# Kernel optimization log

Measured on AMD Instinct MI355X. Metric: run time of the kernel, lower is better.

## Reference

```python
import jax, jax.numpy as jnp
import numpy as np

EPS = 1e-5

def _bn(x, g, b, m, v):
    # eval-mode BatchNorm1d over channel dim of [B, C, T]
    scale = g / jnp.sqrt(v + EPS)
    return (x - m[:, None]) * scale[:, None] + b[:, None]

def _conv3(x, w, b):
    # [B, W, T] conv with kernel [W, W, 3], padding=1
    y = jax.lax.conv_general_dilated(x, w, (1,), [(1, 1)],
                                     dimension_numbers=('NCH', 'OIH', 'NCH'))
    return y + b[None, :, None]

def setup_inputs() -> dict:
    key = jax.random.key(0)
    ks = iter(jax.random.split(key, 32))
    def n(shape, s=0.05):
        return jax.random.normal(next(ks), shape, jnp.float32) * s
    def u(shape):
        return jax.random.uniform(next(ks), shape, jnp.float32, 0.5, 1.5)
    B, T, C, S, W = 128, 4096, 125, 5, 25
    return dict(
        low_freq=jax.random.normal(next(ks), (B, 10, T), jnp.float32),
        w1=n((S, W, 2)), b1=n((S, W)),
        w3=n((S - 1, W, W, 3)), b3=n((S - 1, W)),
        bn_g=jnp.ones((S, W)), bn_b=jnp.zeros((S, W)), bn_m=n((S, W)), bn_v=u((S, W)),
        gw1=n((C // 4, C)), gb1=n((C // 4,)),          # gating Linear(125, 31)
        gw2=n((S, C // 4)), gb2=n((S,)),               # gating Linear(31, 5)
        id_w=n((C, 10)), id_b=n((C,)),                 # identity_proj Conv1d(10,125,1)
        pf_w=n((C, C)), pf_b=n((C,)),                  # proj_final Conv1d(125,125,1)
        fbn_g=jnp.ones((C,)), fbn_b=jnp.zeros((C,)), fbn_m=n((C,)), fbn_v=u((C,)),
        ln_g=jnp.ones((C,)), ln_b=jnp.zeros((C,)),
        fc1_w=n((64, C)), fc1_b=n((64,)),
        fc2_w=n((2, 64)), fc2_b=n((2,)),
    )

def reference(low_freq, w1, b1, w3, b3, bn_g, bn_b, bn_m, bn_v,
              gw1, gb1, gw2, gb2, id_w, id_b, pf_w, pf_b,
              fbn_g, fbn_b, fbn_m, fbn_v, ln_g, ln_b,
              fc1_w, fc1_b, fc2_w, fc2_b):
    S = w1.shape[0]
    B, _, T = low_freq.shape
    identity = jnp.einsum('bct,oc->bot', low_freq, id_w) + id_b[None, :, None]
    chunks = low_freq.reshape(B, S, 2, T)              # torch.chunk over 10 channels
    # all 1x1 convs at once: [S, B, W, T]
    xs = jnp.einsum('bsct,swc->sbwt', chunks, w1) + b1[:, None, :, None]
    y = [None] * S
    y[S - 1] = jax.nn.relu(_bn(xs[S - 1], bn_g[S - 1], bn_b[S - 1], bn_m[S - 1], bn_v[S - 1]))
    for i in range(S - 2, -1, -1):                     # sequential Res2Net recursion
        yi = _conv3(xs[i] + y[i + 1], w3[i], b3[i])
        y[i] = jax.nn.relu(_bn(yi, bn_g[i], bn_b[i], bn_m[i], bn_v[i]))
    ms = jnp.concatenate(y, axis=1)                    # [B, 125, T]
    avg = jnp.mean(ms, axis=-1)                        # [B, 125]
    gate = jax.nn.sigmoid(jax.nn.relu(avg @ gw1.T + gb1) @ gw2.T + gb2)  # [B, S]
    yw = jnp.stack(y, axis=1) * gate[:, :, None, None] # [B, S, W, T]
    gated = yw.reshape(B, -1, T)
    proj = jnp.einsum('bct,oc->bot', gated, pf_w) + pf_b[None, :, None]
    out = jax.nn.relu(_bn(proj + identity, fbn_g, fbn_b, fbn_m, fbn_v))
    pooled = jnp.mean(out, axis=-1)                    # GAP -> [B, 125]
    mu = jnp.mean(pooled, axis=-1, keepdims=True)
    var = jnp.var(pooled, axis=-1, keepdims=True)
    normed = (pooled - mu) / jnp.sqrt(var + EPS) * ln_g + ln_b
    h = normed @ fc1_w.T + fc1_b
    h = jnp.where(h > 0, h, 0.2 * h)                   # LeakyReLU(0.2); dropout = identity (eval)
    return h @ fc2_w.T + fc2_b                         # [B, 2]
```

## Files before the change

kernel.cpp:

```cpp
#include <hip/hip_runtime.h>
#include <stdint.h>

typedef unsigned short u16;
typedef unsigned int   u32;
using short8 = __attribute__((ext_vector_type(8))) short;
using f32x4  = __attribute__((ext_vector_type(4))) float;

__device__ __forceinline__ u16 f2bf(float f){
  u32 u = __builtin_bit_cast(u32, f);
  u = u + 0x7fffu + ((u >> 16) & 1u);
  return (u16)(u >> 16);
}
__device__ __forceinline__ u32 packbf2(float a, float b){
  u32 ua = __builtin_bit_cast(u32, a) + 0x8000u;
  u32 ub = __builtin_bit_cast(u32, b) + 0x8000u;
  return (ua >> 16) | (ub & 0xffff0000u);
}

__global__ void prep_kernel(const float* __restrict__ w3,
                            const float* __restrict__ w1,
                            const float* __restrict__ b1,
                            const float* __restrict__ bng,
                            const float* __restrict__ bnv,
                            u16* __restrict__ convA)
{
  int idx = blockIdx.x*256 + threadIdx.x;
  if (idx >= 4*2*3*64*8) return;
  int j = idx & 7, l = (idx>>3) & 63, frag = idx >> 9;
  int tap = frag % 3, mt = (frag/3) & 1, lay = frag/6;
  int m = mt*16 + (l & 15);
  int k = (l>>4)*8 + j;
  float v = 0.f;
  if (m < 25){
    float a = bng[lay*25+m] * rsqrtf(bnv[lay*25+m] + 1e-5f);
    if (k < 25){
      v = a * w3[((lay*25+m)*25 + k)*3 + tap];
    } else if (k == 25){
      float s = 0.f;
      for (int c = 0; c < 25; ++c) s += w3[((lay*25+m)*25+c)*3+tap] * b1[lay*25+c];
      v = a * s;
    } else if (k <= 27){
      int e = k - 26;
      float s = 0.f;
      for (int c = 0; c < 25; ++c) s += w3[((lay*25+m)*25+c)*3+tap] * w1[(lay*25+c)*2+e];
      v = a * s;
    }
  }
  convA[idx] = f2bf(v);
}

template<int PASS>
__global__ __launch_bounds__(256, (PASS==1) ? 3 : 2)
void pass_kernel(const float* __restrict__ lfg,
                 const float* __restrict__ w1g, const float* __restrict__ b1g,
                 const float* __restrict__ b3g,
                 const float* __restrict__ bng, const float* __restrict__ bnb,
                 const float* __restrict__ bnm, const float* __restrict__ bnv,
                 const u16* __restrict__ convA, const u16* __restrict__ Ab,
                 const float* __restrict__ pfb, const float* __restrict__ idb,
                 const float* __restrict__ fbg, const float* __restrict__ fbb,
                 const float* __restrict__ fbm, const float* __restrict__ fbv,
                 float* __restrict__ outpart)
{
  constexpr int CZ = 66;
  __shared__ __align__(16) u16 zws[4][2][CZ*40];
  __shared__ __align__(16) float cAs[4][32];
  __shared__ __align__(16) float w4as[32], w4bs[32], c4s[32];
  __shared__ float accC[(PASS==1)?160:4];
  __shared__ __align__(16) float AfS[(PASS==2)?128:4], BfS[(PASS==2)?128:4];

  const int tid  = threadIdx.x;
  const int lane = tid & 63, wv = tid >> 6;
  const int q = lane >> 4, c16 = lane & 15;
  const int b = blockIdx.y, blk = blockIdx.x;
  const int s = blk*4 + wv;
  const int tbase = s*32 - 16;

  for (int x = tid; x < 4*2*CZ*20; x += 256) ((u32*)zws)[x] = 0u;
  __syncthreads();
  for (int x = tid; x < 4*2*CZ; x += 256){
    int w = x/(2*CZ), rb = (x/CZ)&1, cz = x%CZ;
    int t = (blk*4+w)*32 - 16 + cz - 1;
    zws[w][rb][cz*40 + 25] = ((unsigned)t < 4096u) ? (u16)0x3F80 : (u16)0;
  }
  if (tid < 128){
    int i = tid >> 5, ch = tid & 31;
    float cc = 0.f;
    if (ch < 25){
      float a = bng[i*25+ch]*rsqrtf(bnv[i*25+ch]+1e-5f);
      cc = (b3g[i*25+ch] - bnm[i*25+ch])*a + bnb[i*25+ch];
    }
    cAs[i][ch] = cc;
  } else if (tid < 160){
    int ch = tid - 128;
    float wa=0.f, wb=0.f, cf=0.f;
    if (ch < 25){
      float a = bng[100+ch]*rsqrtf(bnv[100+ch]+1e-5f);
      wa = a*w1g[(100+ch)*2+0]; wb = a*w1g[(100+ch)*2+1];
      cf = a*b1g[100+ch] + (bnb[100+ch] - bnm[100+ch]*a);
    }
    w4as[ch]=wa; w4bs[ch]=wb; c4s[ch]=cf;
  }
  if constexpr (PASS==1){ if (tid < 160) accC[tid] = 0.f; }
  if constexpr (PASS==2){
    if (tid < 128){
      float fs=0.f, fsh=0.f;
      if (tid < 125){
        fs  = fbg[tid]*rsqrtf(fbv[tid]+1e-5f);
        fsh = (pfb[tid]+idb[tid]-fbm[tid])*fs + fbb[tid];
      }
      AfS[tid]=fs; BfS[tid]=fsh;
    }
  }
  __syncthreads();

  const float* lfb = lfg + b*10*4096;

  u32 lpair[4];
  {
    int t = tbase + lane;
    bool ok = (unsigned)t < 4096u;
    #pragma unroll
    for (int k = 0; k < 4; ++k){
      float a = ok ? lfb[(2*k  )*4096 + t] : 0.f;
      float c = ok ? lfb[(2*k+1)*4096 + t] : 0.f;
      lpair[k] = packbf2(a, c);
    }
  }

  f32x4 pacc[2][8];
  if constexpr (PASS==2){
    #pragma unroll
    for (int n2=0;n2<2;++n2)
      #pragma unroll
      for (int m2=0;m2<8;++m2) pacc[n2][m2] = (f32x4){0.f,0.f,0.f,0.f};
  }

  u16* bufA = zws[wv][0];

  {
    const f32x4 wa0 = *(const f32x4*)&w4as[4*q];
    const f32x4 wa1 = *(const f32x4*)&w4as[16+4*q];
    const f32x4 wb0 = *(const f32x4*)&w4bs[4*q];
    const f32x4 wb1 = *(const f32x4*)&w4bs[16+4*q];
    const f32x4 cf0 = *(const f32x4*)&c4s[4*q];
    const f32x4 cf1 = *(const f32x4*)&c4s[16+4*q];
    float s4[8];
    #pragma unroll
    for (int e=0;e<8;++e) s4[e] = 0.f;
    #pragma unroll
    for (int ct=0; ct<4; ++ct){
      const int wc = 16*ct + c16;
      const int t  = tbase + wc;
      const bool tok = (unsigned)t < 4096u;
      const float l8 = tok ? lfb[8*4096 + t] : 0.f;
      const float l9 = tok ? lfb[9*4096 + t] : 0.f;
      float y0[4], y1[4];
      #pragma unroll
      for (int r=0;r<4;++r){
        float a = fmaxf(wa0[r]*l8 + wb0[r]*l9 + cf0[r], 0.f);
        float c = fmaxf(wa1[r]*l8 + wb1[r]*l9 + cf1[r], 0.f);
        y0[r] = tok ? a : 0.f;
        y1[r] = tok ? c : 0.f;
      }
      if (PASS==1 && (ct==1 || ct==2)){
        #pragma unroll
        for (int r=0;r<4;++r){ s4[r] += y0[r]; s4[4+r] += y1[r]; }
      }
      uint2 w0; w0.x = packbf2(y0[0],y0[1]); w0.y = packbf2(y0[2],y0[3]);
      *(uint2*)&bufA[(wc+1)*40 + 4*q] = w0;
      if (q < 2){
        uint2 w1_; w1_.x = packbf2(y1[0],y1[1]); w1_.y = packbf2(y1[2],y1[3]);
        *(uint2*)&bufA[(wc+1)*40 + 16 + 4*q] = w1_;
      } else if (q == 2){
        bufA[(wc+1)*40 + 24] = f2bf(y1[0]);
      }
    }
    *(u32*)&bufA[(lane+1)*40 + 26] = lpair[3];
    if constexpr (PASS==1){
      #pragma unroll
      for (int e=0;e<8;++e){
        float v = s4[e];
        v += __shfl_xor(v,1); v += __shfl_xor(v,2); v += __shfl_xor(v,4); v += __shfl_xor(v,8);
        if (c16 == 0){
          int ch = (e>>2)*16 + 4*q + (e&3);
          if (ch < 25) atomicAdd(&accC[4*32+ch], v);
        }
      }
    }
  }

  if constexpr (PASS==2){
    {
      short8 Am[8];
      #pragma unroll
      for (int m2=0;m2<8;++m2)
        Am[m2] = *(const short8*)(Ab + b*24576 + ((4*8+m2)*64 + lane)*8);
      #pragma unroll
      for (int n2=0;n2<2;++n2){
        const short8 Bm = *(const short8*)&bufA[(17+16*n2+c16)*40 + 8*q];
        #pragma unroll
        for (int m2=0;m2<8;++m2)
          pacc[n2][m2] = __builtin_amdgcn_mfma_f32_16x16x32_bf16(Am[m2], Bm, pacc[n2][m2],0,0,0);
      }
    }
    {
      short8 Am[8];
      #pragma unroll
      for (int m2=0;m2<8;++m2)
        Am[m2] = *(const short8*)(Ab + b*24576 + ((5*8+m2)*64 + lane)*8);
      #pragma unroll
      for (int n2=0;n2<2;++n2){
        const int t = tbase + 16 + 16*n2 + c16;
        u32 bw[4];
        #pragma unroll
        for (int p=0;p<4;++p){
          int k0 = 8*q + 2*p;
          float v0 = (k0   < 10) ? lfb[k0*4096 + t] : 0.f;
          float v1 = (k0+1 < 10) ? lfb[(k0+1)*4096 + t] : 0.f;
          bw[p] = packbf2(v0, v1);
        }
        const short8 Bm = __builtin_bit_cast(short8, bw);
        #pragma unroll
        for (int m2=0;m2<8;++m2)
          pacc[n2][m2] = __builtin_amdgcn_mfma_f32_16x16x32_bf16(Am[m2], Bm, pacc[n2][m2],0,0,0);
      }
    }
  }

  #pragma unroll
  for (int i = 3; i >= 0; --i){
    u16* src = zws[wv][(3-i)&1];
    u16* dst = zws[wv][(4-i)&1];
    short8 Ac0[3], Ac1[3];
    #pragma unroll
    for (int tp=0;tp<3;++tp){
      Ac0[tp] = *(const short8*)(convA + (((i*2+0)*3+tp)*64 + lane)*8);
      Ac1[tp] = *(const short8*)(convA + (((i*2+1)*3+tp)*64 + lane)*8);
    }
    const f32x4 cc0 = *(const f32x4*)&cAs[i][4*q];
    const f32x4 cc1 = *(const f32x4*)&cAs[i][16+4*q];
    float ysum[8];
    #pragma unroll
    for (int e=0;e<8;++e) ysum[e] = 0.f;

    #pragma unroll
    for (int ct=0; ct<4; ++ct){
      const int wc = 16*ct + c16;
      const u16* p = src + wc*40 + 8*q;
      short8 t0 = *(const short8*)(p);
      short8 t1 = *(const short8*)(p + 40);
      short8 t2 = *(const short8*)(p + 80);
      f32x4 a0 = {0.f,0.f,0.f,0.f}, a1 = {0.f,0.f,0.f,0.f};
      a0 = __builtin_amdgcn_mfma_f32_16x16x32_bf16(Ac0[0], t0, a0, 0,0,0);
      a1 = __builtin_amdgcn_mfma_f32_16x16x32_bf16(Ac1[0], t0, a1, 0,0,0);
      a0 = __builtin_amdgcn_mfma_f32_16x16x32_bf16(Ac0[1], t1, a0, 0,0,0);
      a1 = __builtin_amdgcn_mfma_f32_16x16x32_bf16(Ac1[1], t1, a1, 0,0,0);
      a0 = __builtin_amdgcn_mfma_f32_16x16x32_bf16(Ac0[2], t2, a0, 0,0,0);
      a1 = __builtin_amdgcn_mfma_f32_16x16x32_bf16(Ac1[2], t2, a1, 0,0,0);
      const int t = tbase + wc;
      const bool tok = (unsigned)t < 4096u;
      float y0[4], y1[4];
      #pragma unroll
      for (int r=0;r<4;++r){
        float u0 = fmaxf(a0[r] + cc0[r], 0.f);
        float u1 = fmaxf(a1[r] + cc1[r], 0.f);
        y0[r] = tok ? u0 : 0.f;
        y1[r] = tok ? u1 : 0.f;
      }
      if (PASS==1 && (ct==1 || ct==2)){
        #pragma unroll
        for (int r=0;r<4;++r){ ysum[r] += y0[r]; ysum[4+r] += y1[r]; }
      }
      uint2 w0; w0.x = packbf2(y0[0],y0[1]); w0.y = packbf2(y0[2],y0[3]);
      *(uint2*)&dst[(wc+1)*40 + 4*q] = w0;
      if (q < 2){
        uint2 w1_; w1_.x = packbf2(y1[0],y1[1]); w1_.y = packbf2(y1[2],y1[3]);
        *(uint2*)&dst[(wc+1)*40 + 16 + 4*q] = w1_;
      } else if (q == 2){
        dst[(wc+1)*40 + 24] = f2bf(y1[0]);
      }
    }
    if (i > 0) *(u32*)&dst[(lane+1)*40 + 26] = lpair[i-1];
    if constexpr (PASS==1){
      #pragma unroll
      for (int e=0;e<8;++e){
        float v = ysum[e];
        v += __shfl_xor(v,1); v += __shfl_xor(v,2); v += __shfl_xor(v,4); v += __shfl_xor(v,8);
        if (c16 == 0){
          int ch = (e>>2)*16 + 4*q + (e&3);
          if (ch < 25) atomicAdd(&accC[i*32+ch], v);
        }
      }
    }
    if constexpr (PASS==2){
      short8 Am[8];
      #pragma unroll
      for (int m2=0;m2<8;++m2)
        Am[m2] = *(const short8*)(Ab + b*24576 + ((i*8+m2)*64 + lane)*8);
      #pragma unroll
      for (int n2=0;n2<2;++n2){
        const short8 Bm = *(const short8*)&dst[(17+16*n2+c16)*40 + 8*q];
        #pragma unroll
        for (int m2=0;m2<8;++m2)
          pacc[n2][m2] = __builtin_amdgcn_mfma_f32_16x16x32_bf16(Am[m2], Bm, pacc[n2][m2],0,0,0);
      }
    }
  }

  if constexpr (PASS==1){
    __syncthreads();
    if (tid < 160) outpart[(b*32 + blk)*160 + tid] = accC[tid];
  }
  if constexpr (PASS==2){
    f32x4 ps[8];
    #pragma unroll
    for (int m2=0;m2<8;++m2){
      const f32x4 af = *(const f32x4*)&AfS[m2*16+4*q];
      const f32x4 bf = *(const f32x4*)&BfS[m2*16+4*q];
      #pragma unroll
      for (int r=0;r<4;++r){
        float s2 = fmaxf(pacc[0][m2][r]*af[r] + bf[r], 0.f)
                 + fmaxf(pacc[1][m2][r]*af[r] + bf[r], 0.f);
        s2 += __shfl_xor(s2,1); s2 += __shfl_xor(s2,2); s2 += __shfl_xor(s2,4); s2 += __shfl_xor(s2,8);
        ps[m2][r] = s2;
      }
    }
    if (c16 == 0){
      const int widx = (b*32 + blk)*4 + wv;
      #pragma unroll
      for (int m2=0;m2<8;++m2)
        *(f32x4*)&outpart[widx*128 + m2*16 + 4*q] = ps[m2];
    }
  }
}

__global__ void gate_kernel(const float* __restrict__ partialC,
                            const float* __restrict__ gw1, const float* __restrict__ gb1,
                            const float* __restrict__ gw2, const float* __restrict__ gb2,
                            const float* __restrict__ pf_w, const float* __restrict__ id_w,
                            u16* __restrict__ Ab)
{
  int b = blockIdx.x, tid = threadIdx.x;
  __shared__ float avg[125], h1[31], g[6];
  if (tid < 160){
    float s = 0.f;
    for (int k = 0; k < 32; ++k) s += partialC[(b*32+k)*160 + tid];
    int sc = tid >> 5, ch = tid & 31;
    if (ch < 25) avg[sc*25+ch] = s * (1.f/4096.f);
  }
  __syncthreads();
  if (tid < 31){
    float s = gb1[tid];
    for (int c = 0; c < 125; ++c) s += avg[c] * gw1[tid*125 + c];
    h1[tid] = fmaxf(s, 0.f);
  }
  __syncthreads();
  if (tid < 5){
    float s = gb2[tid];
    for (int j = 0; j < 31; ++j) s += h1[j] * gw2[tid*31 + j];
    g[tid] = 1.f / (1.f + expf(-s));
  }
  if (tid == 5) g[5] = 1.f;
  __syncthreads();
  for (int idx = tid; idx < 24576; idx += 256){
    int j = idx & 7, l = (idx>>3) & 63, mt = (idx>>9) & 7, kt = idx >> 12;
    int m = mt*16 + (l & 15), k = (l>>4)*8 + j;
    float v = 0.f;
    if (m < 125){
      if (kt < 5){ if (k < 25) v = pf_w[m*125 + kt*25 + k] * g[kt]; }
      else       { if (k < 10) v = id_w[m*10 + k]; }
    }
    Ab[b*24576 + idx] = f2bf(v);
  }
}

__global__ void final_kernel(const float* __restrict__ pooledpart,
                             const float* __restrict__ ln_g, const float* __restrict__ ln_b,
                             const float* __restrict__ fc1_w, const float* __restrict__ fc1_b,
                             const float* __restrict__ fc2_w, const float* __restrict__ fc2_b,
                             float* __restrict__ out)
{
  int b = blockIdx.x, tid = threadIdx.x;
  __shared__ float pl[125], nr[125], hh[64], st[2];
  for (int c = tid; c < 125; c += 64){
    float s = 0.f;
    for (int k = 0; k < 128; ++k) s += pooledpart[(b*128+k)*128 + c];
    pl[c] = s * (1.f/4096.f);
  }
  __syncthreads();
  if (tid == 0){
    float mu = 0.f;
    for (int c = 0; c < 125; ++c) mu += pl[c];
    mu /= 125.f;
    float va = 0.f;
    for (int c = 0; c < 125; ++c){ float d = pl[c] - mu; va += d*d; }
    va /= 125.f;
    st[0] = mu; st[1] = rsqrtf(va + 1e-5f);
  }
  __syncthreads();
  for (int c = tid; c < 125; c += 64)
    nr[c] = (pl[c] - st[0]) * st[1] * ln_g[c] + ln_b[c];
  __syncthreads();
  {
    float s = fc1_b[tid];
    for (int c = 0; c < 125; ++c) s += nr[c] * fc1_w[tid*125 + c];
    hh[tid] = (s > 0.f) ? s : 0.2f * s;
  }
  __syncthreads();
  if (tid < 2){
    float s = fc2_b[tid];
    for (int j = 0; j < 64; ++j) s += hh[j] * fc2_w[tid*64 + j];
    out[b*2 + tid] = s;
  }
}

extern "C" void kernel_launch(void* const* d_in, const int* in_sizes, int n_in,
                              void* d_out, int out_size, void* d_ws, size_t ws_size,
                              hipStream_t stream)
{
  const float* lf    = (const float*)d_in[0];
  const float* w1    = (const float*)d_in[1];
  const float* b1    = (const float*)d_in[2];
  const float* w3    = (const float*)d_in[3];
  const float* b3    = (const float*)d_in[4];
  const float* bn_g  = (const float*)d_in[5];
  const float* bn_b  = (const float*)d_in[6];
  const float* bn_m  = (const float*)d_in[7];
  const float* bn_v  = (const float*)d_in[8];
  const float* gw1   = (const float*)d_in[9];
  const float* gb1   = (const float*)d_in[10];
  const float* gw2   = (const float*)d_in[11];
  const float* gb2   = (const float*)d_in[12];
  const float* id_w  = (const float*)d_in[13];
  const float* id_b  = (const float*)d_in[14];
  const float* pf_w  = (const float*)d_in[15];
  const float* pf_b  = (const float*)d_in[16];
  const float* fbn_g = (const float*)d_in[17];
  const float* fbn_b = (const float*)d_in[18];
  const float* fbn_m = (const float*)d_in[19];
  const float* fbn_v = (const float*)d_in[20];
  const float* ln_g  = (const float*)d_in[21];
  const float* ln_b  = (const float*)d_in[22];
  const float* fc1_w = (const float*)d_in[23];
  const float* fc1_b = (const float*)d_in[24];
  const float* fc2_w = (const float*)d_in[25];
  const float* fc2_b = (const float*)d_in[26];

  char* ws = (char*)d_ws;
  float* partialC   = (float*)ws;
  float* pooledpart = (float*)(ws + 2621440);
  u16*   Ab         = (u16*)(ws + 2621440 + 8388608);
  u16*   convA      = (u16*)(ws + 2621440 + 8388608 + 6291456);

  prep_kernel<<<48, 256, 0, stream>>>(w3, w1, b1, bn_g, bn_v, convA);
  pass_kernel<1><<<dim3(32,128), 256, 0, stream>>>(lf, w1, b1, b3, bn_g, bn_b,
      bn_m, bn_v, convA, Ab, pf_b, id_b, fbn_g, fbn_b, fbn_m, fbn_v, partialC);
  gate_kernel<<<128, 256, 0, stream>>>(partialC, gw1, gb1, gw2, gb2, pf_w, id_w, Ab);
  pass_kernel<2><<<dim3(32,128), 256, 0, stream>>>(lf, w1, b1, b3, bn_g, bn_b,
      bn_m, bn_v, convA, Ab, pf_b, id_b, fbn_g, fbn_b, fbn_m, fbn_v, pooledpart);
  final_kernel<<<128, 64, 0, stream>>>(pooledpart, ln_g, ln_b, fc1_w, fc1_b,
      fc2_w, fc2_b, (float*)d_out);
}
```

Measured before the change: 397.2 us.

## Single-buffer conv tiles with register prefetch, block-level pooling, parallel gate and final kernels

Each wave now keeps one LDS tile instead of a ping-pong pair and runs the conv recursion in place. The input fragments are prefetched into registers one column tile ahead, so LDS reads overlap the MFMA chain, and the bias constant is folded into the accumulator init. Pass 1 is asked to fit four blocks per CU instead of three. Pass 2 reduces its pooled sums inside the block through LDS atomics, which shrinks the partial buffer and the work left for the final kernel. The gate kernel is split across six blocks per batch, and the final kernel uses 256 threads with shuffle reductions. The in-place tile relies on wave-synchronous ordering of reads before writes, and the higher occupancy target could cause register spills.

```diff
diff --git a/kernel.cpp b/kernel.cpp
--- a/kernel.cpp
+++ b/kernel.cpp
@@ -50,7 +50,7 @@
 }
 
 template<int PASS>
-__global__ __launch_bounds__(256, (PASS==1) ? 3 : 2)
+__global__ __launch_bounds__(256, (PASS==1) ? 4 : 2)
 void pass_kernel(const float* __restrict__ lfg,
                  const float* __restrict__ w1g, const float* __restrict__ b1g,
                  const float* __restrict__ b3g,
@@ -63,10 +63,11 @@
                  float* __restrict__ outpart)
 {
   constexpr int CZ = 66;
-  __shared__ __align__(16) u16 zws[4][2][CZ*40];
+  __shared__ __align__(16) u16 zws[4][CZ*40];
   __shared__ __align__(16) float cAs[4][32];
   __shared__ __align__(16) float w4as[32], w4bs[32], c4s[32];
   __shared__ float accC[(PASS==1)?160:4];
+  __shared__ float pooled[(PASS==2)?128:4];
   __shared__ __align__(16) float AfS[(PASS==2)?128:4], BfS[(PASS==2)?128:4];
 
   const int tid  = threadIdx.x;
@@ -76,12 +77,12 @@
   const int s = blk*4 + wv;
   const int tbase = s*32 - 16;
 
-  for (int x = tid; x < 4*2*CZ*20; x += 256) ((u32*)zws)[x] = 0u;
-  __syncthreads();
-  for (int x = tid; x < 4*2*CZ; x += 256){
-    int w = x/(2*CZ), rb = (x/CZ)&1, cz = x%CZ;
+  for (int x = tid; x < 4*CZ*20; x += 256) ((u32*)zws)[x] = 0u;
+  __syncthreads();
+  for (int x = tid; x < 4*CZ; x += 256){
+    int w = x/CZ, cz = x%CZ;
     int t = (blk*4+w)*32 - 16 + cz - 1;
-    zws[w][rb][cz*40 + 25] = ((unsigned)t < 4096u) ? (u16)0x3F80 : (u16)0;
+    zws[w][cz*40 + 25] = ((unsigned)t < 4096u) ? (u16)0x3F80 : (u16)0;
   }
   if (tid < 128){
     int i = tid >> 5, ch = tid & 31;
@@ -104,6 +105,7 @@
   if constexpr (PASS==1){ if (tid < 160) accC[tid] = 0.f; }
   if constexpr (PASS==2){
     if (tid < 128){
+      pooled[tid] = 0.f;
       float fs=0.f, fsh=0.f;
       if (tid < 125){
         fs  = fbg[tid]*rsqrtf(fbv[tid]+1e-5f);
@@ -136,7 +138,7 @@
       for (int m2=0;m2<8;++m2) pacc[n2][m2] = (f32x4){0.f,0.f,0.f,0.f};
   }
 
-  u16* bufA = zws[wv][0];
+  u16* z = zws[wv];
 
   {
     const f32x4 wa0 = *(const f32x4*)&w4as[4*q];
@@ -168,15 +170,15 @@
         for (int r=0;r<4;++r){ s4[r] += y0[r]; s4[4+r] += y1[r]; }
       }
       uint2 w0; w0.x = packbf2(y0[0],y0[1]); w0.y = packbf2(y0[2],y0[3]);
-      *(uint2*)&bufA[(wc+1)*40 + 4*q] = w0;
+      *(uint2*)&z[(wc+1)*40 + 4*q] = w0;
       if (q < 2){
         uint2 w1_; w1_.x = packbf2(y1[0],y1[1]); w1_.y = packbf2(y1[2],y1[3]);
-        *(uint2*)&bufA[(wc+1)*40 + 16 + 4*q] = w1_;
+        *(uint2*)&z[(wc+1)*40 + 16 + 4*q] = w1_;
       } else if (q == 2){
-        bufA[(wc+1)*40 + 24] = f2bf(y1[0]);
-      }
-    }
-    *(u32*)&bufA[(lane+1)*40 + 26] = lpair[3];
+        z[(wc+1)*40 + 24] = f2bf(y1[0]);
+      }
+    }
+    *(u32*)&z[(lane+1)*40 + 26] = lpair[3];
     if constexpr (PASS==1){
       #pragma unroll
       for (int e=0;e<8;++e){
@@ -198,7 +200,7 @@
         Am[m2] = *(const short8*)(Ab + b*24576 + ((4*8+m2)*64 + lane)*8);
       #pragma unroll
       for (int n2=0;n2<2;++n2){
-        const short8 Bm = *(const short8*)&bufA[(17+16*n2+c16)*40 + 8*q];
+        const short8 Bm = *(const short8*)&z[(17+16*n2+c16)*40 + 8*q];
         #pragma unroll
         for (int m2=0;m2<8;++m2)
           pacc[n2][m2] = __builtin_amdgcn_mfma_f32_16x16x32_bf16(Am[m2], Bm, pacc[n2][m2],0,0,0);
@@ -230,8 +232,6 @@
 
   #pragma unroll
   for (int i = 3; i >= 0; --i){
-    u16* src = zws[wv][(3-i)&1];
-    u16* dst = zws[wv][(4-i)&1];
     short8 Ac0[3], Ac1[3];
     #pragma unroll
     for (int tp=0;tp<3;++tp){
@@ -244,27 +244,43 @@
     #pragma unroll
     for (int e=0;e<8;++e) ysum[e] = 0.f;
 
+    short8 F0[3], F1[3], F2[3];
+    {
+      const u16* p = z + c16*40 + 8*q;
+      F0[0] = *(const short8*)(p);
+      F0[1] = *(const short8*)(p + 40);
+      F0[2] = *(const short8*)(p + 80);
+      const u16* p1 = z + (16 + c16)*40 + 8*q;
+      F1[0] = *(const short8*)(p1);
+      F1[1] = *(const short8*)(p1 + 40);
+      F1[2] = *(const short8*)(p1 + 80);
+    }
     #pragma unroll
     for (int ct=0; ct<4; ++ct){
+      short8* cur = (ct==0) ? F0 : (ct==1) ? F1 : (ct==2) ? F2 : F0;
+      if (ct < 2){
+        short8* nxt = (ct==0) ? F2 : F0;
+        const u16* p = z + (16*(ct+2) + c16)*40 + 8*q;
+        nxt[0] = *(const short8*)(p);
+        nxt[1] = *(const short8*)(p + 40);
+        nxt[2] = *(const short8*)(p + 80);
+      }
+      __builtin_amdgcn_sched_barrier(0);
+      f32x4 a0 = cc0, a1 = cc1;
+      a0 = __builtin_amdgcn_mfma_f32_16x16x32_bf16(Ac0[0], cur[0], a0, 0,0,0);
+      a1 = __builtin_amdgcn_mfma_f32_16x16x32_bf16(Ac1[0], cur[0], a1, 0,0,0);
+      a0 = __builtin_amdgcn_mfma_f32_16x16x32_bf16(Ac0[1], cur[1], a0, 0,0,0);
+      a1 = __builtin_amdgcn_mfma_f32_16x16x32_bf16(Ac1[1], cur[1], a1, 0,0,0);
+      a0 = __builtin_amdgcn_mfma_f32_16x16x32_bf16(Ac0[2], cur[2], a0, 0,0,0);
+      a1 = __builtin_amdgcn_mfma_f32_16x16x32_bf16(Ac1[2], cur[2], a1, 0,0,0);
       const int wc = 16*ct + c16;
-      const u16* p = src + wc*40 + 8*q;
-      short8 t0 = *(const short8*)(p);
-      short8 t1 = *(const short8*)(p + 40);
-      short8 t2 = *(const short8*)(p + 80);
-      f32x4 a0 = {0.f,0.f,0.f,0.f}, a1 = {0.f,0.f,0.f,0.f};
-      a0 = __builtin_amdgcn_mfma_f32_16x16x32_bf16(Ac0[0], t0, a0, 0,0,0);
-      a1 = __builtin_amdgcn_mfma_f32_16x16x32_bf16(Ac1[0], t0, a1, 0,0,0);
-      a0 = __builtin_amdgcn_mfma_f32_16x16x32_bf16(Ac0[1], t1, a0, 0,0,0);
-      a1 = __builtin_amdgcn_mfma_f32_16x16x32_bf16(Ac1[1], t1, a1, 0,0,0);
-      a0 = __builtin_amdgcn_mfma_f32_16x16x32_bf16(Ac0[2], t2, a0, 0,0,0);
-      a1 = __builtin_amdgcn_mfma_f32_16x16x32_bf16(Ac1[2], t2, a1, 0,0,0);
-      const int t = tbase + wc;
+      const int t  = tbase + wc;
       const bool tok = (unsigned)t < 4096u;
       float y0[4], y1[4];
       #pragma unroll
       for (int r=0;r<4;++r){
-        float u0 = fmaxf(a0[r] + cc0[r], 0.f);
-        float u1 = fmaxf(a1[r] + cc1[r], 0.f);
+        float u0 = fmaxf(a0[r], 0.f);
+        float u1 = fmaxf(a1[r], 0.f);
         y0[r] = tok ? u0 : 0.f;
         y1[r] = tok ? u1 : 0.f;
       }
@@ -273,15 +289,15 @@
         for (int r=0;r<4;++r){ ysum[r] += y0[r]; ysum[4+r] += y1[r]; }
       }
       uint2 w0; w0.x = packbf2(y0[0],y0[1]); w0.y = packbf2(y0[2],y0[3]);
-      *(uint2*)&dst[(wc+1)*40 + 4*q] = w0;
+      *(uint2*)&z[(wc+1)*40 + 4*q] = w0;
       if (q < 2){
         uint2 w1_; w1_.x = packbf2(y1[0],y1[1]); w1_.y = packbf2(y1[2],y1[3]);
-        *(uint2*)&dst[(wc+1)*40 + 16 + 4*q] = w1_;
+        *(uint2*)&z[(wc+1)*40 + 16 + 4*q] = w1_;
       } else if (q == 2){
-        dst[(wc+1)*40 + 24] = f2bf(y1[0]);
-      }
-    }
-    if (i > 0) *(u32*)&dst[(lane+1)*40 + 26] = lpair[i-1];
+        z[(wc+1)*40 + 24] = f2bf(y1[0]);
+      }
+    }
+    if (i > 0) *(u32*)&z[(lane+1)*40 + 26] = lpair[i-1];
     if constexpr (PASS==1){
       #pragma unroll
       for (int e=0;e<8;++e){
@@ -300,7 +316,7 @@
         Am[m2] = *(const short8*)(Ab + b*24576 + ((i*8+m2)*64 + lane)*8);
       #pragma unroll
       for (int n2=0;n2<2;++n2){
-        const short8 Bm = *(const short8*)&dst[(17+16*n2+c16)*40 + 8*q];
+        const short8 Bm = *(const short8*)&z[(17+16*n2+c16)*40 + 8*q];
         #pragma unroll
         for (int m2=0;m2<8;++m2)
           pacc[n2][m2] = __builtin_amdgcn_mfma_f32_16x16x32_bf16(Am[m2], Bm, pacc[n2][m2],0,0,0);
@@ -313,7 +329,6 @@
     if (tid < 160) outpart[(b*32 + blk)*160 + tid] = accC[tid];
   }
   if constexpr (PASS==2){
-    f32x4 ps[8];
     #pragma unroll
     for (int m2=0;m2<8;++m2){
       const f32x4 af = *(const f32x4*)&AfS[m2*16+4*q];
@@ -323,15 +338,11 @@
         float s2 = fmaxf(pacc[0][m2][r]*af[r] + bf[r], 0.f)
                  + fmaxf(pacc[1][m2][r]*af[r] + bf[r], 0.f);
         s2 += __shfl_xor(s2,1); s2 += __shfl_xor(s2,2); s2 += __shfl_xor(s2,4); s2 += __shfl_xor(s2,8);
-        ps[m2][r] = s2;
-      }
-    }
-    if (c16 == 0){
-      const int widx = (b*32 + blk)*4 + wv;
-      #pragma unroll
-      for (int m2=0;m2<8;++m2)
-        *(f32x4*)&outpart[widx*128 + m2*16 + 4*q] = ps[m2];
-    }
+        if (c16 == 0) atomicAdd(&pooled[m2*16 + 4*q + r], s2);
+      }
+    }
+    __syncthreads();
+    if (tid < 128) outpart[(b*32 + blk)*128 + tid] = pooled[tid];
   }
 }
 
@@ -341,7 +352,7 @@
                             const float* __restrict__ pf_w, const float* __restrict__ id_w,
                             u16* __restrict__ Ab)
 {
-  int b = blockIdx.x, tid = threadIdx.x;
+  int b = blockIdx.x, kt = blockIdx.y, tid = threadIdx.x;
   __shared__ float avg[125], h1[31], g[6];
   if (tid < 160){
     float s = 0.f;
@@ -363,15 +374,16 @@
   }
   if (tid == 5) g[5] = 1.f;
   __syncthreads();
-  for (int idx = tid; idx < 24576; idx += 256){
-    int j = idx & 7, l = (idx>>3) & 63, mt = (idx>>9) & 7, kt = idx >> 12;
+  const float gk = g[kt];
+  for (int x = tid; x < 4096; x += 256){
+    int j = x & 7, l = (x>>3) & 63, mt = (x>>9) & 7;
     int m = mt*16 + (l & 15), k = (l>>4)*8 + j;
     float v = 0.f;
     if (m < 125){
-      if (kt < 5){ if (k < 25) v = pf_w[m*125 + kt*25 + k] * g[kt]; }
+      if (kt < 5){ if (k < 25) v = pf_w[m*125 + kt*25 + k] * gk; }
       else       { if (k < 10) v = id_w[m*10 + k]; }
     }
-    Ab[b*24576 + idx] = f2bf(v);
+    Ab[b*24576 + kt*4096 + x] = f2bf(v);
   }
 }
 
@@ -382,30 +394,44 @@
                              float* __restrict__ out)
 {
   int b = blockIdx.x, tid = threadIdx.x;
-  __shared__ float pl[125], nr[125], hh[64], st[2];
-  for (int c = tid; c < 125; c += 64){
+  __shared__ float ps[2][128], pl[128], nr[128], hh[64], st[2];
+  {
+    int c = tid & 127, h = tid >> 7;
     float s = 0.f;
-    for (int k = 0; k < 128; ++k) s += pooledpart[(b*128+k)*128 + c];
-    pl[c] = s * (1.f/4096.f);
-  }
-  __syncthreads();
-  if (tid == 0){
-    float mu = 0.f;
-    for (int c = 0; c < 125; ++c) mu += pl[c];
-    mu /= 125.f;
-    float va = 0.f;
-    for (int c = 0; c < 125; ++c){ float d = pl[c] - mu; va += d*d; }
-    va /= 125.f;
-    st[0] = mu; st[1] = rsqrtf(va + 1e-5f);
-  }
-  __syncthreads();
-  for (int c = tid; c < 125; c += 64)
-    nr[c] = (pl[c] - st[0]) * st[1] * ln_g[c] + ln_b[c];
+    for (int k = h*16; k < h*16+16; ++k) s += pooledpart[(b*32+k)*128 + c];
+    ps[h][c] = s;
+  }
+  __syncthreads();
+  if (tid < 128) pl[tid] = (ps[0][tid] + ps[1][tid]) * (1.f/4096.f);
+  __syncthreads();
+  if (tid < 64){
+    float v0 = (tid < 125) ? pl[tid] : 0.f;
+    float v1 = (tid+64 < 125) ? pl[tid+64] : 0.f;
+    float sm = v0 + v1;
+    #pragma unroll
+    for (int o = 1; o < 64; o <<= 1) sm += __shfl_xor(sm, o);
+    float mu = sm * (1.f/125.f);
+    float d0 = (tid < 125) ? (pl[tid]-mu) : 0.f;
+    float d1 = (tid+64 < 125) ? (pl[tid+64]-mu) : 0.f;
+    float sv = d0*d0 + d1*d1;
+    #pragma unroll
+    for (int o = 1; o < 64; o <<= 1) sv += __shfl_xor(sv, o);
+    if (tid == 0){ st[0] = mu; st[1] = rsqrtf(sv*(1.f/125.f) + 1e-5f); }
+  }
+  __syncthreads();
+  if (tid < 125) nr[tid] = (pl[tid] - st[0]) * st[1] * ln_g[tid] + ln_b[tid];
+  else if (tid < 128) nr[tid] = 0.f;
   __syncthreads();
   {
-    float s = fc1_b[tid];
-    for (int c = 0; c < 125; ++c) s += nr[c] * fc1_w[tid*125 + c];
-    hh[tid] = (s > 0.f) ? s : 0.2f * s;
+    int u = tid >> 2, part = tid & 3;
+    float s = 0.f;
+    for (int c = part*32; c < part*32+32 && c < 125; ++c)
+      s += nr[c] * fc1_w[u*125 + c];
+    s += __shfl_xor(s, 1); s += __shfl_xor(s, 2);
+    if (part == 0){
+      float h = s + fc1_b[u];
+      hh[u] = (h > 0.f) ? h : 0.2f*h;
+    }
   }
   __syncthreads();
   if (tid < 2){
@@ -450,15 +476,16 @@
   char* ws = (char*)d_ws;
   float* partialC   = (float*)ws;
   float* pooledpart = (float*)(ws + 2621440);
-  u16*   Ab         = (u16*)(ws + 2621440 + 8388608);
-  u16*   convA      = (u16*)(ws + 2621440 + 8388608 + 6291456);
+  u16*   Ab         = (u16*)(ws + 2621440 + 2097152);
+  u16*   convA      = (u16*)(ws + 2621440 + 2097152 + 6291456);
 
   prep_kernel<<<48, 256, 0, stream>>>(w3, w1, b1, bn_g, bn_v, convA);
   pass_kernel<1><<<dim3(32,128), 256, 0, stream>>>(lf, w1, b1, b3, bn_g, bn_b,
       bn_m, bn_v, convA, Ab, pf_b, id_b, fbn_g, fbn_b, fbn_m, fbn_v, partialC);
-  gate_kernel<<<128, 256, 0, stream>>>(partialC, gw1, gb1, gw2, gb2, pf_w, id_w, Ab);
+  gate_kernel<<<dim3(128,6), 256, 0, stream>>>(partialC, gw1, gb1, gw2, gb2,
+      pf_w, id_w, Ab);
   pass_kernel<2><<<dim3(32,128), 256, 0, stream>>>(lf, w1, b1, b3, bn_g, bn_b,
       bn_m, bn_v, convA, Ab, pf_b, id_b, fbn_g, fbn_b, fbn_m, fbn_v, pooledpart);
-  final_kernel<<<128, 64, 0, stream>>>(pooledpart, ln_g, ln_b, fc1_w, fc1_b,
+  final_kernel<<<128, 256, 0, stream>>>(pooledpart, ln_g, ln_b, fc1_w, fc1_b,
       fc2_w, fc2_b, (float*)d_out);
 }
```

Result: faster. 377.4 us (-5.0%).
